# Optimization experiments

Measured on AMD Instinct MI355X. Metric: run time of the kernel, lower is better.

The kernel has to match this reference:

```python
import jax, jax.numpy as jnp
import numpy as np

N_NODES = 100000
N_EDGES = 1600000


def setup_inputs() -> dict:
    key = jax.random.key(0)
    ks = jax.random.split(key, 6)
    x = jax.random.normal(ks[0], (N_NODES, 128), dtype=jnp.float32)
    edge_index = jax.random.randint(ks[1], (2, N_EDGES), 0, N_NODES, dtype=jnp.int64)
    # glorot-ish scaled weights
    W0 = jax.random.normal(ks[2], (128, 64), dtype=jnp.float32) * (1.0 / np.sqrt(128))
    W1 = jax.random.normal(ks[3], (64, 64), dtype=jnp.float32) * (1.0 / np.sqrt(64))
    W2 = jax.random.normal(ks[4], (64, 40), dtype=jnp.float32) * (1.0 / np.sqrt(64))
    b0 = jnp.zeros((64,), jnp.float32)
    b1 = jnp.zeros((64,), jnp.float32)
    b2 = jnp.zeros((40,), jnp.float32)
    return {"x": x, "edge_index": edge_index, "W0": W0, "b0": b0,
            "W1": W1, "b1": b1, "W2": W2, "b2": b2}


def _gcn_norm(edge_index, n, dtype):
    # PyG gcn_norm: add self-loops, deg over targets, norm = d^-1/2[src]*d^-1/2[dst]
    loop = jnp.arange(n, dtype=edge_index.dtype)
    src = jnp.concatenate([edge_index[0], loop])
    dst = jnp.concatenate([edge_index[1], loop])
    deg = jax.ops.segment_sum(jnp.ones_like(dst, dtype=dtype), dst, num_segments=n)
    dinv = jnp.where(deg > 0, jax.lax.rsqrt(deg), 0.0)
    return src, dst, dinv[src] * dinv[dst]


def reference(x, edge_index, W0, b0, W1, b1, W2, b2):
    n = x.shape[0]
    src, dst, norm = _gcn_norm(edge_index, n, x.dtype)

    def conv(h, W, b):
        h = h @ W                                   # [N, out]
        msg = h[src] * norm[:, None]                # gather + per-edge scale
        return jax.ops.segment_sum(msg, dst, num_segments=n) + b

    # dropout skipped (eval mode); relu between layers per forward()
    h = jax.nn.relu(conv(x, W0, b0))
    h = jax.nn.relu(conv(h, W1, b1))
    return conv(h, W2, b2)
```

## Files before the change

kernel.cpp:

```cpp
#include <hip/hip_runtime.h>
#include <hip/hip_fp16.h>


#define ALIGN256(x) (((size_t)(x) + 255) & ~(size_t)255)


__global__ __launch_bounds__(256) void k_coarse(const int* __restrict__ ei,
                                                int* __restrict__ ccnt,
                                                int E, int NBUK) {
    __shared__ int h[512];
    int t = threadIdx.x;
    for (int i = t; i < NBUK; i += 256) h[i] = 0;
    __syncthreads();
    int e0 = blockIdx.x * 8192;
    int e1 = min(e0 + 8192, E);
    for (int e = e0 + t; e < e1; e += 256) atomicAdd(&h[ei[E + e] >> 8], 1);
    __syncthreads();
    for (int i = t; i < NBUK; i += 256) {
        int c = h[i];
        if (c) atomicAdd(&ccnt[i], c);
    }
}


__global__ __launch_bounds__(256) void k_cscan(const int* __restrict__ ccnt,
                                               int* __restrict__ cbase,
                                               int* __restrict__ cpos,
                                               int* __restrict__ row_start,
                                               int NBUK, int E, int N) {
    __shared__ int sd[256];
    int t = threadIdx.x;
    int i0 = 2 * t, i1 = 2 * t + 1;
    int v0 = (i0 < NBUK) ? ccnt[i0] : 0;
    int v1 = (i1 < NBUK) ? ccnt[i1] : 0;
    int s = v0 + v1;
    sd[t] = s;
    __syncthreads();
    for (int off = 1; off < 256; off <<= 1) {
        int u = (t >= off) ? sd[t - off] : 0;
        __syncthreads();
        sd[t] += u;
        __syncthreads();
    }
    int base = sd[t] - s;
    if (i0 < NBUK) { cbase[i0] = base;      cpos[i0] = base; }
    if (i1 < NBUK) { cbase[i1] = base + v0; cpos[i1] = base + v0; }
    if (t == 0) { cbase[NBUK] = E; row_start[N] = E; }
}


__global__ __launch_bounds__(256) void k_passA(const int* __restrict__ ei,
                                               int* __restrict__ cpos,
                                               unsigned int* __restrict__ stage,
                                               int E, int NBUK) {
    __shared__ int h[512];
    __shared__ int base[512];
    int t = threadIdx.x;
    for (int i = t; i < NBUK; i += 256) h[i] = 0;
    __syncthreads();
    int e0 = blockIdx.x * 8192;
    int e1 = min(e0 + 8192, E);
    for (int e = e0 + t; e < e1; e += 256) atomicAdd(&h[ei[E + e] >> 8], 1);
    __syncthreads();
    for (int b = t; b < NBUK; b += 256) {
        int c = h[b];
        base[b] = c ? atomicAdd(&cpos[b], c) : 0;
        h[b] = 0;
    }
    __syncthreads();
    for (int e = e0 + t; e < e1; e += 256) {
        unsigned int s = (unsigned int)ei[e];
        int d = ei[E + e];
        int b = d >> 8;
        int off = base[b] + atomicAdd(&h[b], 1);
        stage[off] = ((unsigned int)(d & 255) << 24) | s;
    }
}


__global__ __launch_bounds__(256) void k_B1(const unsigned int* __restrict__ stage,
                                            const int* __restrict__ cbase,
                                            int* __restrict__ row_start,
                                            float* __restrict__ dinv, int N) {
    __shared__ int cnt[256];
    __shared__ int sd[256];
    int b = blockIdx.x;
    int n0 = b << 8;
    int t = threadIdx.x;
    cnt[t] = 0;
    __syncthreads();
    int s0 = cbase[b], s1 = cbase[b + 1];
    for (int j = s0 + t; j < s1; j += 256) atomicAdd(&cnt[stage[j] >> 24], 1);
    __syncthreads();
    int c = cnt[t];
    sd[t] = c;
    __syncthreads();
    for (int off = 1; off < 256; off <<= 1) {
        int u = (t >= off) ? sd[t - off] : 0;
        __syncthreads();
        sd[t] += u;
        __syncthreads();
    }
    int excl = sd[t] - c;
    int node = n0 + t;
    if (node < N) {
        row_start[node] = s0 + excl;
        dinv[node] = 1.0f / sqrtf((float)(c + 1));
    }
}


__global__ __launch_bounds__(256) void k_B2(const unsigned int* __restrict__ stage,
                                            const int* __restrict__ cbase,
                                            const int* __restrict__ row_start,
                                            const float* __restrict__ dinv,
                                            int2* __restrict__ ep, int N) {
    __shared__ int lpos[256];
    __shared__ float ld[256];
    int b = blockIdx.x;
    int n0 = b << 8;
    int t = threadIdx.x;
    int node = n0 + t;
    if (node < N) {
        lpos[t] = row_start[node];
        ld[t] = dinv[node];
    }
    __syncthreads();
    int s0 = cbase[b], s1 = cbase[b + 1];
    for (int j = s0 + t; j < s1; j += 256) {
        unsigned int v = stage[j];
        int li = v >> 24;
        int src = v & 0xFFFFFF;
        int slot = atomicAdd(&lpos[li], 1);
        ep[slot] = make_int2(src, __float_as_int(dinv[src] * ld[li]));
    }
}


template <int K, int OUT>
__global__ __launch_bounds__(256) void k_gemm32(const float* __restrict__ X,
                                                const float* __restrict__ W,
                                                __half* __restrict__ Y, int N) {
    __shared__ float Wl[32 * 64];
    __shared__ float Al[64 * 36];
    int tid = threadIdx.x;
    int tx = tid & 15;
    int ty = tid >> 4;
    int row0 = blockIdx.x * 64;

    float acc[4][4];
#pragma unroll
    for (int i = 0; i < 4; i++)
#pragma unroll
        for (int j = 0; j < 4; j++) acc[i][j] = 0.0f;

    for (int kt = 0; kt < K; kt += 32) {
        __syncthreads();
#pragma unroll
        for (int it = 0; it < 2; it++) {
            int idx = tid + it * 256;
            int k = idx >> 4;
            int c4 = (idx & 15) << 2;
            float4 v = make_float4(0.f, 0.f, 0.f, 0.f);
            if (c4 < OUT) v = *(const float4*)&W[(size_t)(kt + k) * OUT + c4];
            *(float4*)&Wl[k * 64 + c4] = v;
        }
#pragma unroll
        for (int it = 0; it < 2; it++) {
            int vid = tid + it * 256;
            int r = vid >> 3;
            int kk = (vid & 7) << 2;
            int row = row0 + r;
            float4 v = make_float4(0.f, 0.f, 0.f, 0.f);
            if (row < N) v = *(const float4*)&X[(size_t)row * K + kt + kk];
            *(float4*)&Al[r * 36 + kk] = v;
        }
        __syncthreads();
#pragma unroll
        for (int k = 0; k < 32; k += 4) {
            float4 a[4], w[4];
#pragma unroll
            for (int i = 0; i < 4; i++) a[i] = *(const float4*)&Al[(ty + 16 * i) * 36 + k];
#pragma unroll
            for (int j = 0; j < 4; j++) w[j] = *(const float4*)&Wl[(k + j) * 64 + 4 * tx];
#pragma unroll
            for (int i = 0; i < 4; i++) {
                acc[i][0] += a[i].x * w[0].x; acc[i][1] += a[i].x * w[0].y;
                acc[i][2] += a[i].x * w[0].z; acc[i][3] += a[i].x * w[0].w;
                acc[i][0] += a[i].y * w[1].x; acc[i][1] += a[i].y * w[1].y;
                acc[i][2] += a[i].y * w[1].z; acc[i][3] += a[i].y * w[1].w;
                acc[i][0] += a[i].z * w[2].x; acc[i][1] += a[i].z * w[2].y;
                acc[i][2] += a[i].z * w[2].z; acc[i][3] += a[i].z * w[2].w;
                acc[i][0] += a[i].w * w[3].x; acc[i][1] += a[i].w * w[3].y;
                acc[i][2] += a[i].w * w[3].z; acc[i][3] += a[i].w * w[3].w;
            }
        }
    }

    int c0 = 4 * tx;
#pragma unroll
    for (int i = 0; i < 4; i++) {
        int row = row0 + ty + 16 * i;
        if (row < N && c0 + 4 <= OUT) {
            __half2 p0 = __floats2half2_rn(acc[i][0], acc[i][1]);
            __half2 p1 = __floats2half2_rn(acc[i][2], acc[i][3]);
            uint2 pk = make_uint2(*(unsigned int*)&p0, *(unsigned int*)&p1);
            *(uint2*)&Y[(size_t)row * OUT + c0] = pk;
        }
    }
}


template <int OUT>
__global__ __launch_bounds__(256) void k_gemm16(const __half* __restrict__ X,
                                                const float* __restrict__ W,
                                                __half* __restrict__ Y, int N) {
    __shared__ float Wl[32 * 64];
    __shared__ float Al[64 * 36];
    int tid = threadIdx.x;
    int tx = tid & 15;
    int ty = tid >> 4;
    int row0 = blockIdx.x * 64;

    float acc[4][4];
#pragma unroll
    for (int i = 0; i < 4; i++)
#pragma unroll
        for (int j = 0; j < 4; j++) acc[i][j] = 0.0f;

    for (int kt = 0; kt < 64; kt += 32) {
        __syncthreads();
#pragma unroll
        for (int it = 0; it < 2; it++) {
            int idx = tid + it * 256;
            int k = idx >> 4;
            int c4 = (idx & 15) << 2;
            float4 v = make_float4(0.f, 0.f, 0.f, 0.f);
            if (c4 < OUT) v = *(const float4*)&W[(size_t)(kt + k) * OUT + c4];
            *(float4*)&Wl[k * 64 + c4] = v;
        }
#pragma unroll
        for (int it = 0; it < 2; it++) {
            int vid = tid + it * 256;
            int r = vid >> 3;
            int kk = (vid & 7) << 2;
            int row = row0 + r;
            uint2 hv = make_uint2(0, 0);
            if (row < N) hv = *(const uint2*)&X[(size_t)row * 64 + kt + kk];
            __half2* hp = (__half2*)&hv;
            float2 f0 = __half22float2(hp[0]);
            float2 f1 = __half22float2(hp[1]);
            *(float4*)&Al[r * 36 + kk] = make_float4(f0.x, f0.y, f1.x, f1.y);
        }
        __syncthreads();
#pragma unroll
        for (int k = 0; k < 32; k += 4) {
            float4 a[4], w[4];
#pragma unroll
            for (int i = 0; i < 4; i++) a[i] = *(const float4*)&Al[(ty + 16 * i) * 36 + k];
#pragma unroll
            for (int j = 0; j < 4; j++) w[j] = *(const float4*)&Wl[(k + j) * 64 + 4 * tx];
#pragma unroll
            for (int i = 0; i < 4; i++) {
                acc[i][0] += a[i].x * w[0].x; acc[i][1] += a[i].x * w[0].y;
                acc[i][2] += a[i].x * w[0].z; acc[i][3] += a[i].x * w[0].w;
                acc[i][0] += a[i].y * w[1].x; acc[i][1] += a[i].y * w[1].y;
                acc[i][2] += a[i].y * w[1].z; acc[i][3] += a[i].y * w[1].w;
                acc[i][0] += a[i].z * w[2].x; acc[i][1] += a[i].z * w[2].y;
                acc[i][2] += a[i].z * w[2].z; acc[i][3] += a[i].z * w[2].w;
                acc[i][0] += a[i].w * w[3].x; acc[i][1] += a[i].w * w[3].y;
                acc[i][2] += a[i].w * w[3].z; acc[i][3] += a[i].w * w[3].w;
            }
        }
    }

    int c0 = 4 * tx;
#pragma unroll
    for (int i = 0; i < 4; i++) {
        int row = row0 + ty + 16 * i;
        if (row < N && c0 + 4 <= OUT) {
            __half2 p0 = __floats2half2_rn(acc[i][0], acc[i][1]);
            __half2 p1 = __floats2half2_rn(acc[i][2], acc[i][3]);
            uint2 pk = make_uint2(*(unsigned int*)&p0, *(unsigned int*)&p1);
            *(uint2*)&Y[(size_t)row * OUT + c0] = pk;
        }
    }
}


__device__ __forceinline__ void fma8(float4& a0, float4& a1, uint4 hv, float w) {
    __half2* hp = (__half2*)&hv;
    float2 f0 = __half22float2(hp[0]);
    float2 f1 = __half22float2(hp[1]);
    float2 f2 = __half22float2(hp[2]);
    float2 f3 = __half22float2(hp[3]);
    a0.x += f0.x * w; a0.y += f0.y * w; a0.z += f1.x * w; a0.w += f1.y * w;
    a1.x += f2.x * w; a1.y += f2.y * w; a1.z += f3.x * w; a1.w += f3.y * w;
}

template <int NV, int F, int RELU, typename OutT>
__global__ __launch_bounds__(256) void k_agg(const __half* __restrict__ H,
                                             const int* __restrict__ row_start,
                                             const int2* __restrict__ ep,
                                             const float* __restrict__ dinv,
                                             const float* __restrict__ bias,
                                             OutT* __restrict__ out, int N) {
    int tid = threadIdx.x;
    int lane = tid & 63;
    int sub = lane >> 3;
    int lq = lane & 7;
    int node = blockIdx.x * 32 + (tid >> 6) * 8 + sub;
    if (node >= N) return;
    const bool act = (NV == 8) || (lq < NV);

    int jb = row_start[node];
    int je = row_start[node + 1];
    float dv = dinv[node];

    float4 a0 = make_float4(0.f, 0.f, 0.f, 0.f);
    float4 a1 = make_float4(0.f, 0.f, 0.f, 0.f);
    if (act) {
        uint4 hv = *(const uint4*)&H[(size_t)node * F + 8 * lq];
        fma8(a0, a1, hv, dv * dv);
    }

    int j = jb;
    for (; j + 8 <= je; j += 8) {
        int2 e0 = ep[j],     e1 = ep[j + 1], e2 = ep[j + 2], e3 = ep[j + 3];
        int2 e4 = ep[j + 4], e5 = ep[j + 5], e6 = ep[j + 6], e7 = ep[j + 7];
        if (act) {
            uint4 h0 = *(const uint4*)&H[(size_t)e0.x * F + 8 * lq];
            uint4 h1 = *(const uint4*)&H[(size_t)e1.x * F + 8 * lq];
            uint4 h2 = *(const uint4*)&H[(size_t)e2.x * F + 8 * lq];
            uint4 h3 = *(const uint4*)&H[(size_t)e3.x * F + 8 * lq];
            uint4 h4 = *(const uint4*)&H[(size_t)e4.x * F + 8 * lq];
            uint4 h5 = *(const uint4*)&H[(size_t)e5.x * F + 8 * lq];
            uint4 h6 = *(const uint4*)&H[(size_t)e6.x * F + 8 * lq];
            uint4 h7 = *(const uint4*)&H[(size_t)e7.x * F + 8 * lq];
            fma8(a0, a1, h0, __int_as_float(e0.y));
            fma8(a0, a1, h1, __int_as_float(e1.y));
            fma8(a0, a1, h2, __int_as_float(e2.y));
            fma8(a0, a1, h3, __int_as_float(e3.y));
            fma8(a0, a1, h4, __int_as_float(e4.y));
            fma8(a0, a1, h5, __int_as_float(e5.y));
            fma8(a0, a1, h6, __int_as_float(e6.y));
            fma8(a0, a1, h7, __int_as_float(e7.y));
        }
    }
    for (; j + 2 <= je; j += 2) {
        int2 e0 = ep[j], e1 = ep[j + 1];
        if (act) {
            uint4 h0 = *(const uint4*)&H[(size_t)e0.x * F + 8 * lq];
            uint4 h1 = *(const uint4*)&H[(size_t)e1.x * F + 8 * lq];
            fma8(a0, a1, h0, __int_as_float(e0.y));
            fma8(a0, a1, h1, __int_as_float(e1.y));
        }
    }
    if (j < je) {
        int2 e = ep[j];
        if (act) {
            uint4 h = *(const uint4*)&H[(size_t)e.x * F + 8 * lq];
            fma8(a0, a1, h, __int_as_float(e.y));
        }
    }

    if (act) {
        float4 b0 = *(const float4*)&bias[8 * lq];
        float4 b1 = *(const float4*)&bias[8 * lq + 4];
        a0.x += b0.x; a0.y += b0.y; a0.z += b0.z; a0.w += b0.w;
        a1.x += b1.x; a1.y += b1.y; a1.z += b1.z; a1.w += b1.w;
        if (RELU) {
            a0.x = fmaxf(a0.x, 0.f); a0.y = fmaxf(a0.y, 0.f);
            a0.z = fmaxf(a0.z, 0.f); a0.w = fmaxf(a0.w, 0.f);
            a1.x = fmaxf(a1.x, 0.f); a1.y = fmaxf(a1.y, 0.f);
            a1.z = fmaxf(a1.z, 0.f); a1.w = fmaxf(a1.w, 0.f);
        }
        if constexpr (sizeof(OutT) == 2) {
            __half2 p0 = __floats2half2_rn(a0.x, a0.y);
            __half2 p1 = __floats2half2_rn(a0.z, a0.w);
            __half2 p2 = __floats2half2_rn(a1.x, a1.y);
            __half2 p3 = __floats2half2_rn(a1.z, a1.w);
            uint4 pk = make_uint4(*(unsigned int*)&p0, *(unsigned int*)&p1,
                                  *(unsigned int*)&p2, *(unsigned int*)&p3);
            *(uint4*)&out[(size_t)node * F + 8 * lq] = pk;
        } else {
            *(float4*)&out[(size_t)node * F + 8 * lq] = a0;
            *(float4*)&out[(size_t)node * F + 8 * lq + 4] = a1;
        }
    }
}


extern "C" void kernel_launch(void* const* d_in, const int* in_sizes, int n_in,
                              void* d_out, int out_size, void* d_ws, size_t ws_size,
                              hipStream_t stream) {
    const float* x  = (const float*)d_in[0];
    const int*   ei = (const int*)d_in[1];
    const float* W0 = (const float*)d_in[2];
    const float* b0 = (const float*)d_in[3];
    const float* W1 = (const float*)d_in[4];
    const float* b1 = (const float*)d_in[5];
    const float* W2 = (const float*)d_in[6];
    const float* b2 = (const float*)d_in[7];
    float* out = (float*)d_out;

    const int N = in_sizes[0] / 128;
    const int E = in_sizes[1] / 2;
    const int NBUK = (N + 255) >> 8;

    char* w = (char*)d_ws;
    size_t off = 0;
    int*    ccnt      = (int*)(w + off);    off = ALIGN256(off + (size_t)NBUK * 4);
    int*    cbase     = (int*)(w + off);    off = ALIGN256(off + (size_t)(NBUK + 1) * 4);
    int*    cpos      = (int*)(w + off);    off = ALIGN256(off + (size_t)NBUK * 4);
    int*    row_start = (int*)(w + off);    off = ALIGN256(off + (size_t)(N + 1) * 4);
    float*  dinv      = (float*)(w + off);  off = ALIGN256(off + (size_t)N * 4);
    int2*   ep        = (int2*)(w + off);   off = ALIGN256(off + (size_t)E * 8);
    __half* bufH      = (__half*)(w + off); off = ALIGN256(off + (size_t)N * 64 * 2);
    __half* bufG      = (__half*)(w + off); off = ALIGN256(off + (size_t)N * 64 * 2);
    unsigned int* stage = (unsigned int*)bufG;

    const int gGemm = (N + 63) / 64;
    const int gAgg  = (N + 31) / 32;
    const int gPA   = (E + 8191) / 8192;

    hipMemsetAsync(ccnt, 0, (size_t)NBUK * 4, stream);
    k_gemm32<128, 64><<<gGemm, 256, 0, stream>>>(x, W0, bufH, N);
    k_coarse<<<gPA, 256, 0, stream>>>(ei, ccnt, E, NBUK);
    k_cscan<<<1, 256, 0, stream>>>(ccnt, cbase, cpos, row_start, NBUK, E, N);
    k_passA<<<gPA, 256, 0, stream>>>(ei, cpos, stage, E, NBUK);
    k_B1<<<NBUK, 256, 0, stream>>>(stage, cbase, row_start, dinv, N);
    k_B2<<<NBUK, 256, 0, stream>>>(stage, cbase, row_start, dinv, ep, N);

    k_agg<8, 64, 1, __half><<<gAgg, 256, 0, stream>>>(bufH, row_start, ep, dinv, b0, bufG, N);
    k_gemm16<64><<<gGemm, 256, 0, stream>>>(bufG, W1, bufH, N);
    k_agg<8, 64, 1, __half><<<gAgg, 256, 0, stream>>>(bufH, row_start, ep, dinv, b1, bufG, N);
    k_gemm16<40><<<gGemm, 256, 0, stream>>>(bufG, W2, bufH, N);
    k_agg<5, 40, 0, float><<<gAgg, 256, 0, stream>>>(bufH, row_start, ep, dinv, b2, out, N);
}
```

Measured before the change: 326.0 us.

## Fuse aggregation with following GEMM and merge coarse histogram into first GEMM

Each hidden-layer aggregation (gather, bias, ReLU) now writes its 64-row tile into shared memory as fp32, and the next layer's GEMM reads it from there. This removes the fp16 round trip through global memory and two kernel launches. The coarse bucket histogram runs as extra blocks of the first GEMM launch, removing another launch. The cost is more shared memory per block and less aggregation parallelism: 8 lanes per node, two nodes per thread group, with 64-row blocks.

```diff
diff --git a/kernel.cpp b/kernel.cpp
--- a/kernel.cpp
+++ b/kernel.cpp
@@ -3,24 +3,6 @@
 
 
 #define ALIGN256(x) (((size_t)(x) + 255) & ~(size_t)255)
-
-
-__global__ __launch_bounds__(256) void k_coarse(const int* __restrict__ ei,
-                                                int* __restrict__ ccnt,
-                                                int E, int NBUK) {
-    __shared__ int h[512];
-    int t = threadIdx.x;
-    for (int i = t; i < NBUK; i += 256) h[i] = 0;
-    __syncthreads();
-    int e0 = blockIdx.x * 8192;
-    int e1 = min(e0 + 8192, E);
-    for (int e = e0 + t; e < e1; e += 256) atomicAdd(&h[ei[E + e] >> 8], 1);
-    __syncthreads();
-    for (int i = t; i < NBUK; i += 256) {
-        int c = h[i];
-        if (c) atomicAdd(&ccnt[i], c);
-    }
-}
 
 
 __global__ __launch_bounds__(256) void k_cscan(const int* __restrict__ ccnt,
@@ -140,10 +122,30 @@
 template <int K, int OUT>
 __global__ __launch_bounds__(256) void k_gemm32(const float* __restrict__ X,
                                                 const float* __restrict__ W,
-                                                __half* __restrict__ Y, int N) {
+                                                __half* __restrict__ Y, int N,
+                                                int gemmBlocks,
+                                                const int* __restrict__ ei,
+                                                int* __restrict__ ccnt, int E) {
     __shared__ float Wl[32 * 64];
     __shared__ float Al[64 * 36];
     int tid = threadIdx.x;
+
+    if ((int)blockIdx.x >= gemmBlocks) {
+        int* h = (int*)Wl;
+        int NBUK = (N + 255) >> 8;
+        for (int i = tid; i < NBUK; i += 256) h[i] = 0;
+        __syncthreads();
+        int e0 = (blockIdx.x - gemmBlocks) * 8192;
+        int e1 = min(e0 + 8192, E);
+        for (int e = e0 + tid; e < e1; e += 256) atomicAdd(&h[ei[E + e] >> 8], 1);
+        __syncthreads();
+        for (int i = tid; i < NBUK; i += 256) {
+            int c = h[i];
+            if (c) atomicAdd(&ccnt[i], c);
+        }
+        return;
+    }
+
     int tx = tid & 15;
     int ty = tid >> 4;
     int row0 = blockIdx.x * 64;
@@ -211,17 +213,90 @@
 }
 
 
+__device__ __forceinline__ void fma8(float4& a0, float4& a1, uint4 hv, float w) {
+    __half2* hp = (__half2*)&hv;
+    float2 f0 = __half22float2(hp[0]);
+    float2 f1 = __half22float2(hp[1]);
+    float2 f2 = __half22float2(hp[2]);
+    float2 f3 = __half22float2(hp[3]);
+    a0.x += f0.x * w; a0.y += f0.y * w; a0.z += f1.x * w; a0.w += f1.y * w;
+    a1.x += f2.x * w; a1.y += f2.y * w; a1.z += f3.x * w; a1.w += f3.y * w;
+}
+
+
 template <int OUT>
-__global__ __launch_bounds__(256) void k_gemm16(const __half* __restrict__ X,
-                                                const float* __restrict__ W,
-                                                __half* __restrict__ Y, int N) {
+__global__ __launch_bounds__(256) void k_agg_gemm(const __half* __restrict__ H,
+                                                  const int* __restrict__ row_start,
+                                                  const int2* __restrict__ ep,
+                                                  const float* __restrict__ dinv,
+                                                  const float* __restrict__ bias,
+                                                  const float* __restrict__ W,
+                                                  __half* __restrict__ Y, int N) {
+    __shared__ float Af[64 * 68];
     __shared__ float Wl[32 * 64];
-    __shared__ float Al[64 * 36];
     int tid = threadIdx.x;
+    int lq = tid & 7;
+    int sg = tid >> 3;
+    int row0 = blockIdx.x * 64;
+
+#pragma unroll
+    for (int half = 0; half < 2; half++) {
+        int r = sg + 32 * half;
+        int node = row0 + r;
+        float4 a0 = make_float4(0.f, 0.f, 0.f, 0.f);
+        float4 a1 = make_float4(0.f, 0.f, 0.f, 0.f);
+        if (node < N) {
+            int jb = row_start[node];
+            int je = row_start[node + 1];
+            float dv = dinv[node];
+            uint4 hv = *(const uint4*)&H[(size_t)node * 64 + 8 * lq];
+            fma8(a0, a1, hv, dv * dv);
+            int j = jb;
+            for (; j + 8 <= je; j += 8) {
+                int2 e0 = ep[j],     e1 = ep[j + 1], e2 = ep[j + 2], e3 = ep[j + 3];
+                int2 e4 = ep[j + 4], e5 = ep[j + 5], e6 = ep[j + 6], e7 = ep[j + 7];
+                uint4 h0 = *(const uint4*)&H[(size_t)e0.x * 64 + 8 * lq];
+                uint4 h1 = *(const uint4*)&H[(size_t)e1.x * 64 + 8 * lq];
+                uint4 h2 = *(const uint4*)&H[(size_t)e2.x * 64 + 8 * lq];
+                uint4 h3 = *(const uint4*)&H[(size_t)e3.x * 64 + 8 * lq];
+                uint4 h4 = *(const uint4*)&H[(size_t)e4.x * 64 + 8 * lq];
+                uint4 h5 = *(const uint4*)&H[(size_t)e5.x * 64 + 8 * lq];
+                uint4 h6 = *(const uint4*)&H[(size_t)e6.x * 64 + 8 * lq];
+                uint4 h7 = *(const uint4*)&H[(size_t)e7.x * 64 + 8 * lq];
+                fma8(a0, a1, h0, __int_as_float(e0.y));
+                fma8(a0, a1, h1, __int_as_float(e1.y));
+                fma8(a0, a1, h2, __int_as_float(e2.y));
+                fma8(a0, a1, h3, __int_as_float(e3.y));
+                fma8(a0, a1, h4, __int_as_float(e4.y));
+                fma8(a0, a1, h5, __int_as_float(e5.y));
+                fma8(a0, a1, h6, __int_as_float(e6.y));
+                fma8(a0, a1, h7, __int_as_float(e7.y));
+            }
+            for (; j + 2 <= je; j += 2) {
+                int2 e0 = ep[j], e1 = ep[j + 1];
+                uint4 h0 = *(const uint4*)&H[(size_t)e0.x * 64 + 8 * lq];
+                uint4 h1 = *(const uint4*)&H[(size_t)e1.x * 64 + 8 * lq];
+                fma8(a0, a1, h0, __int_as_float(e0.y));
+                fma8(a0, a1, h1, __int_as_float(e1.y));
+            }
+            if (j < je) {
+                int2 e = ep[j];
+                uint4 h = *(const uint4*)&H[(size_t)e.x * 64 + 8 * lq];
+                fma8(a0, a1, h, __int_as_float(e.y));
+            }
+            float4 b0v = *(const float4*)&bias[8 * lq];
+            float4 b1v = *(const float4*)&bias[8 * lq + 4];
+            a0.x = fmaxf(a0.x + b0v.x, 0.f); a0.y = fmaxf(a0.y + b0v.y, 0.f);
+            a0.z = fmaxf(a0.z + b0v.z, 0.f); a0.w = fmaxf(a0.w + b0v.w, 0.f);
+            a1.x = fmaxf(a1.x + b1v.x, 0.f); a1.y = fmaxf(a1.y + b1v.y, 0.f);
+            a1.z = fmaxf(a1.z + b1v.z, 0.f); a1.w = fmaxf(a1.w + b1v.w, 0.f);
+        }
+        *(float4*)&Af[r * 68 + 8 * lq] = a0;
+        *(float4*)&Af[r * 68 + 8 * lq + 4] = a1;
+    }
+
     int tx = tid & 15;
     int ty = tid >> 4;
-    int row0 = blockIdx.x * 64;
-
     float acc[4][4];
 #pragma unroll
     for (int i = 0; i < 4; i++)
@@ -239,25 +314,12 @@
             if (c4 < OUT) v = *(const float4*)&W[(size_t)(kt + k) * OUT + c4];
             *(float4*)&Wl[k * 64 + c4] = v;
         }
-#pragma unroll
-        for (int it = 0; it < 2; it++) {
-            int vid = tid + it * 256;
-            int r = vid >> 3;
-            int kk = (vid & 7) << 2;
-            int row = row0 + r;
-            uint2 hv = make_uint2(0, 0);
-            if (row < N) hv = *(const uint2*)&X[(size_t)row * 64 + kt + kk];
-            __half2* hp = (__half2*)&hv;
-            float2 f0 = __half22float2(hp[0]);
-            float2 f1 = __half22float2(hp[1]);
-            *(float4*)&Al[r * 36 + kk] = make_float4(f0.x, f0.y, f1.x, f1.y);
-        }
         __syncthreads();
 #pragma unroll
         for (int k = 0; k < 32; k += 4) {
             float4 a[4], w[4];
 #pragma unroll
-            for (int i = 0; i < 4; i++) a[i] = *(const float4*)&Al[(ty + 16 * i) * 36 + k];
+            for (int i = 0; i < 4; i++) a[i] = *(const float4*)&Af[(ty + 16 * i) * 68 + kt + k];
 #pragma unroll
             for (int j = 0; j < 4; j++) w[j] = *(const float4*)&Wl[(k + j) * 64 + 4 * tx];
 #pragma unroll
@@ -288,23 +350,13 @@
 }
 
 
-__device__ __forceinline__ void fma8(float4& a0, float4& a1, uint4 hv, float w) {
-    __half2* hp = (__half2*)&hv;
-    float2 f0 = __half22float2(hp[0]);
-    float2 f1 = __half22float2(hp[1]);
-    float2 f2 = __half22float2(hp[2]);
-    float2 f3 = __half22float2(hp[3]);
-    a0.x += f0.x * w; a0.y += f0.y * w; a0.z += f1.x * w; a0.w += f1.y * w;
-    a1.x += f2.x * w; a1.y += f2.y * w; a1.z += f3.x * w; a1.w += f3.y * w;
-}
-
-template <int NV, int F, int RELU, typename OutT>
+template <int NV, int F, int RELU>
 __global__ __launch_bounds__(256) void k_agg(const __half* __restrict__ H,
                                              const int* __restrict__ row_start,
                                              const int2* __restrict__ ep,
                                              const float* __restrict__ dinv,
                                              const float* __restrict__ bias,
-                                             OutT* __restrict__ out, int N) {
+                                             float* __restrict__ out, int N) {
     int tid = threadIdx.x;
     int lane = tid & 63;
     int sub = lane >> 3;
@@ -375,18 +427,8 @@
             a1.x = fmaxf(a1.x, 0.f); a1.y = fmaxf(a1.y, 0.f);
             a1.z = fmaxf(a1.z, 0.f); a1.w = fmaxf(a1.w, 0.f);
         }
-        if constexpr (sizeof(OutT) == 2) {
-            __half2 p0 = __floats2half2_rn(a0.x, a0.y);
-            __half2 p1 = __floats2half2_rn(a0.z, a0.w);
-            __half2 p2 = __floats2half2_rn(a1.x, a1.y);
-            __half2 p3 = __floats2half2_rn(a1.z, a1.w);
-            uint4 pk = make_uint4(*(unsigned int*)&p0, *(unsigned int*)&p1,
-                                  *(unsigned int*)&p2, *(unsigned int*)&p3);
-            *(uint4*)&out[(size_t)node * F + 8 * lq] = pk;
-        } else {
-            *(float4*)&out[(size_t)node * F + 8 * lq] = a0;
-            *(float4*)&out[(size_t)node * F + 8 * lq + 4] = a1;
-        }
+        *(float4*)&out[(size_t)node * F + 8 * lq] = a0;
+        *(float4*)&out[(size_t)node * F + 8 * lq + 4] = a1;
     }
 }
 
@@ -425,16 +467,13 @@
     const int gPA   = (E + 8191) / 8192;
 
     hipMemsetAsync(ccnt, 0, (size_t)NBUK * 4, stream);
-    k_gemm32<128, 64><<<gGemm, 256, 0, stream>>>(x, W0, bufH, N);
-    k_coarse<<<gPA, 256, 0, stream>>>(ei, ccnt, E, NBUK);
+    k_gemm32<128, 64><<<gGemm + gPA, 256, 0, stream>>>(x, W0, bufH, N, gGemm, ei, ccnt, E);
     k_cscan<<<1, 256, 0, stream>>>(ccnt, cbase, cpos, row_start, NBUK, E, N);
     k_passA<<<gPA, 256, 0, stream>>>(ei, cpos, stage, E, NBUK);
     k_B1<<<NBUK, 256, 0, stream>>>(stage, cbase, row_start, dinv, N);
     k_B2<<<NBUK, 256, 0, stream>>>(stage, cbase, row_start, dinv, ep, N);
 
-    k_agg<8, 64, 1, __half><<<gAgg, 256, 0, stream>>>(bufH, row_start, ep, dinv, b0, bufG, N);
-    k_gemm16<64><<<gGemm, 256, 0, stream>>>(bufG, W1, bufH, N);
-    k_agg<8, 64, 1, __half><<<gAgg, 256, 0, stream>>>(bufH, row_start, ep, dinv, b1, bufG, N);
-    k_gemm16<40><<<gGemm, 256, 0, stream>>>(bufG, W2, bufH, N);
-    k_agg<5, 40, 0, float><<<gAgg, 256, 0, stream>>>(bufH, row_start, ep, dinv, b2, out, N);
-}
+    k_agg_gemm<64><<<gGemm, 256, 0, stream>>>(bufH, row_start, ep, dinv, b0, W1, bufG, N);
+    k_agg_gemm<40><<<gGemm, 256, 0, stream>>>(bufG, row_start, ep, dinv, b1, W2, bufH, N);
+    k_agg<5, 40, 0><<<gAgg, 256, 0, stream>>>(bufH, row_start, ep, dinv, b2, out, N);
+}
```

Measured after the change: 425.2 us. +30.4%, slower.

## Fuse coarse bucket histogram into first GEMM launch, drop memset

Applied to the files above, without the earlier changes.

Adds extra blocks to the first GEMM kernel that compute per-slice coarse destination-bucket histograms in shared memory and write them out without global atomics. The scan kernel then sums the per-slice histograms itself. This removes a memset and a separate kernel launch and lets the histogram work overlap with the GEMM. In exchange, the scan does serial per-slice reads, and the histogram blocks can shape how the fused kernel's blocks are scheduled.

```diff
diff --git a/kernel.cpp b/kernel.cpp
--- a/kernel.cpp
+++ b/kernel.cpp
@@ -4,26 +4,11 @@
 
 #define ALIGN256(x) (((size_t)(x) + 255) & ~(size_t)255)
 
-
-__global__ __launch_bounds__(256) void k_coarse(const int* __restrict__ ei,
-                                                int* __restrict__ ccnt,
-                                                int E, int NBUK) {
-    __shared__ int h[512];
-    int t = threadIdx.x;
-    for (int i = t; i < NBUK; i += 256) h[i] = 0;
-    __syncthreads();
-    int e0 = blockIdx.x * 8192;
-    int e1 = min(e0 + 8192, E);
-    for (int e = e0 + t; e < e1; e += 256) atomicAdd(&h[ei[E + e] >> 8], 1);
-    __syncthreads();
-    for (int i = t; i < NBUK; i += 256) {
-        int c = h[i];
-        if (c) atomicAdd(&ccnt[i], c);
-    }
-}
-
-
-__global__ __launch_bounds__(256) void k_cscan(const int* __restrict__ ccnt,
+#define HEDGE 32768
+
+
+__global__ __launch_bounds__(256) void k_cscan(const int* __restrict__ hist,
+                                               int nslices,
                                                int* __restrict__ cbase,
                                                int* __restrict__ cpos,
                                                int* __restrict__ row_start,
@@ -31,8 +16,9 @@
     __shared__ int sd[256];
     int t = threadIdx.x;
     int i0 = 2 * t, i1 = 2 * t + 1;
-    int v0 = (i0 < NBUK) ? ccnt[i0] : 0;
-    int v1 = (i1 < NBUK) ? ccnt[i1] : 0;
+    int v0 = 0, v1 = 0;
+    if (i0 < NBUK) for (int b = 0; b < nslices; b++) v0 += hist[b * NBUK + i0];
+    if (i1 < NBUK) for (int b = 0; b < nslices; b++) v1 += hist[b * NBUK + i1];
     int s = v0 + v1;
     sd[t] = s;
     __syncthreads();
@@ -140,10 +126,28 @@
 template <int K, int OUT>
 __global__ __launch_bounds__(256) void k_gemm32(const float* __restrict__ X,
                                                 const float* __restrict__ W,
-                                                __half* __restrict__ Y, int N) {
+                                                __half* __restrict__ Y, int N,
+                                                int gemmBlocks,
+                                                const int* __restrict__ ei,
+                                                int* __restrict__ hist, int E) {
     __shared__ float Wl[32 * 64];
     __shared__ float Al[64 * 36];
     int tid = threadIdx.x;
+
+    if ((int)blockIdx.x >= gemmBlocks) {
+        int* h = (int*)Wl;
+        int NBUK = (N + 255) >> 8;
+        int slice = blockIdx.x - gemmBlocks;
+        for (int i = tid; i < NBUK; i += 256) h[i] = 0;
+        __syncthreads();
+        int e0 = slice * HEDGE;
+        int e1 = min(e0 + HEDGE, E);
+        for (int e = e0 + tid; e < e1; e += 256) atomicAdd(&h[ei[E + e] >> 8], 1);
+        __syncthreads();
+        for (int i = tid; i < NBUK; i += 256) hist[slice * NBUK + i] = h[i];
+        return;
+    }
+
     int tx = tid & 15;
     int ty = tid >> 4;
     int row0 = blockIdx.x * 64;
@@ -407,10 +411,11 @@
     const int N = in_sizes[0] / 128;
     const int E = in_sizes[1] / 2;
     const int NBUK = (N + 255) >> 8;
+    const int NSL  = (E + HEDGE - 1) / HEDGE;
 
     char* w = (char*)d_ws;
     size_t off = 0;
-    int*    ccnt      = (int*)(w + off);    off = ALIGN256(off + (size_t)NBUK * 4);
+    int*    hist      = (int*)(w + off);    off = ALIGN256(off + (size_t)NSL * NBUK * 4);
     int*    cbase     = (int*)(w + off);    off = ALIGN256(off + (size_t)(NBUK + 1) * 4);
     int*    cpos      = (int*)(w + off);    off = ALIGN256(off + (size_t)NBUK * 4);
     int*    row_start = (int*)(w + off);    off = ALIGN256(off + (size_t)(N + 1) * 4);
@@ -424,10 +429,8 @@
     const int gAgg  = (N + 31) / 32;
     const int gPA   = (E + 8191) / 8192;
 
-    hipMemsetAsync(ccnt, 0, (size_t)NBUK * 4, stream);
-    k_gemm32<128, 64><<<gGemm, 256, 0, stream>>>(x, W0, bufH, N);
-    k_coarse<<<gPA, 256, 0, stream>>>(ei, ccnt, E, NBUK);
-    k_cscan<<<1, 256, 0, stream>>>(ccnt, cbase, cpos, row_start, NBUK, E, N);
+    k_gemm32<128, 64><<<gGemm + NSL, 256, 0, stream>>>(x, W0, bufH, N, gGemm, ei, hist, E);
+    k_cscan<<<1, 256, 0, stream>>>(hist, NSL, cbase, cpos, row_start, NBUK, E, N);
     k_passA<<<gPA, 256, 0, stream>>>(ei, cpos, stage, E, NBUK);
     k_B1<<<NBUK, 256, 0, stream>>>(stage, cbase, row_start, dinv, N);
     k_B2<<<NBUK, 256, 0, stream>>>(stage, cbase, row_start, dinv, ep, N);
```

New measurement: 347.0 us. +6.4%, slower.
